# Kernel optimization log

Hardware: AMD Instinct MI355X
Metric: run time of the kernel (lower is better)

Reference implementation:

```python
import jax, jax.numpy as jnp
import numpy as np

NUM_EXPERTS = 64


def setup_inputs() -> dict:
    key = jax.random.key(0)
    k1, k2 = jax.random.split(key)
    x = jax.random.normal(k1, (4, 4096, 2048), dtype=jnp.float32)
    # nn.Linear default init scale ~ 1/sqrt(dim); exact init irrelevant for correctness
    gate_w = jax.random.normal(k2, (NUM_EXPERTS, 2048), dtype=jnp.float32) * (1.0 / np.sqrt(2048.0))
    expert_bias = jnp.zeros((NUM_EXPERTS,), dtype=jnp.float32)
    return {"x": x, "gate_w": gate_w, "expert_bias": expert_bias, "top_k": 8}


def reference(x, gate_w, expert_bias, top_k):
    # x: [B, S, D]; gate_w: [E, D]; expert_bias: [E]
    B, S, D = x.shape
    x_flat = x.reshape(-1, D)                                  # [T, D], T = B*S
    logits = jnp.einsum('td,ed->te', x_flat, gate_w) + expert_bias  # [T, E]
    top_k_logits, top_k_indices = jax.lax.top_k(logits, top_k)      # [T, K]
    top_k_weights = jax.nn.softmax(top_k_logits, axis=-1)           # [T, K]
    # training-mode load counting (scatter_add over expert ids)
    expert_counts = jax.ops.segment_sum(
        jnp.ones((B * S * top_k,), dtype=jnp.float32),
        top_k_indices.reshape(-1),
        num_segments=NUM_EXPERTS,
    )                                                               # [E]
    return top_k_indices, top_k_weights, expert_counts
```

## Files before the change

### kernel.cpp

```cpp
#include <hip/hip_runtime.h>
#include <math.h>

#define T_TOKENS 16384
#define D_DIM    2048
#define E_EXP    64
#define TOPK     8
#define NS       8
#define NCH      (D_DIM / NS / 32)

typedef __attribute__((ext_vector_type(8))) short bf16x8;
typedef __attribute__((ext_vector_type(4))) float f32x4;

__device__ __forceinline__ unsigned short bf16rne(float f) {
  unsigned u = __builtin_bit_cast(unsigned, f);
  unsigned r = u + 0x7fffu + ((u >> 16) & 1u);
  return (unsigned short)(r >> 16);
}
__device__ __forceinline__ float bf16f(unsigned short h) {
  return __builtin_bit_cast(float, (unsigned)h << 16);
}

__device__ __forceinline__ void split8(const float4 v0, const float4 v1,
                                       bf16x8& hi, bf16x8& lo) {
  const float xs[8] = {v0.x, v0.y, v0.z, v0.w, v1.x, v1.y, v1.z, v1.w};
  #pragma unroll
  for (int j = 0; j < 8; ++j) {
    unsigned short h = bf16rne(xs[j]);
    hi[j] = (short)h;
    lo[j] = (short)bf16rne(xs[j] - bf16f(h));
  }
}

__global__ __launch_bounds__(256) void convert_g_kernel(
    const float* __restrict__ gw, unsigned short* __restrict__ ph,
    unsigned short* __restrict__ pl, float* __restrict__ counts_zero)
{
  const int id = blockIdx.x * 256 + threadIdx.x;
  if (blockIdx.x == 0 && threadIdx.x < E_EXP) counts_zero[threadIdx.x] = 0.0f;

  const int e  = id & 63;
  const int kq = (id >> 6) & 3;
  const int c  = id >> 8;
  const float* gp = &gw[(size_t)e * D_DIM + c * 32 + kq * 8];
  float4 v0 = *(const float4*)&gp[0];
  float4 v1 = *(const float4*)&gp[4];
  bf16x8 hi, lo;
  split8(v0, v1, hi, lo);
  *(bf16x8*)&ph[(size_t)id * 8] = hi;
  *(bf16x8*)&pl[(size_t)id * 8] = lo;
}

__global__ __launch_bounds__(256, 4) void moe_logits_kernel(
    const float* __restrict__ x, const unsigned short* __restrict__ ph,
    const unsigned short* __restrict__ pl, float* __restrict__ part)
{
  const int tid  = threadIdx.x;
  const int wave = tid >> 6;
  const int lane = tid & 63;
  const int l15  = lane & 15;
  const int quad = lane >> 4;
  const int ks   = blockIdx.y;
  const int k0   = ks * (D_DIM / NS);
  const int tokw = blockIdx.x * 128 + wave * 32;

  f32x4 acc[2][4];
  #pragma unroll
  for (int s = 0; s < 2; ++s)
    #pragma unroll
    for (int et = 0; et < 4; ++et) acc[s][et] = (f32x4){0.f, 0.f, 0.f, 0.f};

  const float* xp0 = &x[(size_t)(tokw + l15)      * D_DIM + k0 + quad * 8];
  const float* xp1 = &x[(size_t)(tokw + 16 + l15) * D_DIM + k0 + quad * 8];
  const unsigned short* bp_h = &ph[(((size_t)(k0 >> 5) * 4 + quad) * 64 + l15) * 8];
  const unsigned short* bp_l = &pl[(((size_t)(k0 >> 5) * 4 + quad) * 64 + l15) * 8];

  float4 a0 = *(const float4*)&xp0[0], a1 = *(const float4*)&xp0[4];
  float4 b0 = *(const float4*)&xp1[0], b1 = *(const float4*)&xp1[4];

  #pragma unroll 1
  for (int c = 0; c < NCH; ++c) {
    float4 na0, na1, nb0, nb1;
    if (c + 1 < NCH) {
      const float* q0 = xp0 + (c + 1) * 32;
      const float* q1 = xp1 + (c + 1) * 32;
      na0 = *(const float4*)&q0[0]; na1 = *(const float4*)&q0[4];
      nb0 = *(const float4*)&q1[0]; nb1 = *(const float4*)&q1[4];
    }

    bf16x8 ah0, al0, ah1, al1;
    split8(a0, a1, ah0, al0);
    split8(b0, b1, ah1, al1);

    const unsigned short* ch = bp_h + (size_t)c * 2048;
    const unsigned short* cl = bp_l + (size_t)c * 2048;
    #pragma unroll
    for (int et = 0; et < 4; ++et) {
      bf16x8 bh = *(const bf16x8*)&ch[et * 128];
      bf16x8 bl = *(const bf16x8*)&cl[et * 128];
      acc[0][et] = __builtin_amdgcn_mfma_f32_16x16x32_bf16(ah0, bh, acc[0][et], 0, 0, 0);
      acc[0][et] = __builtin_amdgcn_mfma_f32_16x16x32_bf16(ah0, bl, acc[0][et], 0, 0, 0);
      acc[0][et] = __builtin_amdgcn_mfma_f32_16x16x32_bf16(al0, bh, acc[0][et], 0, 0, 0);
      acc[0][et] = __builtin_amdgcn_mfma_f32_16x16x32_bf16(al0, bl, acc[0][et], 0, 0, 0);
      acc[1][et] = __builtin_amdgcn_mfma_f32_16x16x32_bf16(ah1, bh, acc[1][et], 0, 0, 0);
      acc[1][et] = __builtin_amdgcn_mfma_f32_16x16x32_bf16(ah1, bl, acc[1][et], 0, 0, 0);
      acc[1][et] = __builtin_amdgcn_mfma_f32_16x16x32_bf16(al1, bh, acc[1][et], 0, 0, 0);
      acc[1][et] = __builtin_amdgcn_mfma_f32_16x16x32_bf16(al1, bl, acc[1][et], 0, 0, 0);
    }

    a0 = na0; a1 = na1; b0 = nb0; b1 = nb1;
  }

  #pragma unroll
  for (int sub = 0; sub < 2; ++sub) {
    #pragma unroll
    for (int et = 0; et < 4; ++et) {
      #pragma unroll
      for (int r = 0; r < 4; ++r) {
        const size_t t = (size_t)tokw + sub * 16 + quad * 4 + r;
        part[((size_t)ks * T_TOKENS + t) * E_EXP + et * 16 + l15] = acc[sub][et][r];
      }
    }
  }
}

__global__ __launch_bounds__(64) void topk_kernel(
    const float* __restrict__ part, const float* __restrict__ bias,
    float* __restrict__ out)
{
  __shared__ unsigned hist[E_EXP];
  const int tid = threadIdx.x;
  const int t = blockIdx.x * 64 + tid;
  hist[tid] = 0;
  __syncthreads();

  float l[E_EXP];
  #pragma unroll
  for (int j = 0; j < E_EXP / 4; ++j) {
    float4 b = *(const float4*)&bias[j * 4];
    l[4*j] = b.x; l[4*j+1] = b.y; l[4*j+2] = b.z; l[4*j+3] = b.w;
  }
  #pragma unroll 1
  for (int ks = 0; ks < NS; ++ks) {
    const float4* p = (const float4*)&part[((size_t)ks * T_TOKENS + t) * E_EXP];
    #pragma unroll
    for (int j = 0; j < E_EXP / 4; ++j) {
      float4 v = p[j];
      l[4*j] += v.x; l[4*j+1] += v.y; l[4*j+2] += v.z; l[4*j+3] += v.w;
    }
  }

  float tv[TOPK]; int tix[TOPK];
  unsigned long long used = 0ull;
  #pragma unroll
  for (int k = 0; k < TOPK; ++k) {
    float best = -INFINITY; int bi = 0;
    #pragma unroll
    for (int j = 0; j < E_EXP; ++j) {
      bool ok = (((used >> j) & 1ull) == 0ull) && (l[j] > best);
      best = ok ? l[j] : best;
      bi   = ok ? j : bi;
    }
    tv[k] = best; tix[k] = bi;
    used |= (1ull << bi);
  }

  float m = tv[0], s = 0.0f, w[TOPK];
  #pragma unroll
  for (int k = 0; k < TOPK; ++k) { w[k] = expf(tv[k] - m); s += w[k]; }
  float inv = 1.0f / s;

  #pragma unroll
  for (int k = 0; k < TOPK; ++k) {
    out[(size_t)t * TOPK + k] = (float)tix[k];
    out[(size_t)T_TOKENS * TOPK + (size_t)t * TOPK + k] = w[k] * inv;
  }

  #pragma unroll
  for (int k = 0; k < TOPK; ++k) atomicAdd(&hist[tix[k]], 1u);
  __syncthreads();
  atomicAdd(&out[2 * (size_t)T_TOKENS * TOPK + tid], (float)hist[tid]);
}

extern "C" void kernel_launch(void* const* d_in, const int* in_sizes, int n_in,
                              void* d_out, int out_size, void* d_ws, size_t ws_size,
                              hipStream_t stream) {
  const float* x    = (const float*)d_in[0];
  const float* gw   = (const float*)d_in[1];
  const float* bias = (const float*)d_in[2];
  float* out  = (float*)d_out;

  float* part = (float*)d_ws;
  const size_t part_elems = (size_t)NS * T_TOKENS * E_EXP;
  unsigned short* ph = (unsigned short*)((char*)d_ws + part_elems * sizeof(float));
  unsigned short* pl = ph + (size_t)E_EXP * D_DIM;

  convert_g_kernel<<<dim3(E_EXP * D_DIM / 8 / 256), dim3(256), 0, stream>>>(
      gw, ph, pl, out + 2 * (size_t)T_TOKENS * TOPK);
  moe_logits_kernel<<<dim3(T_TOKENS / 128, NS), dim3(256), 0, stream>>>(
      x, ph, pl, part);
  topk_kernel<<<dim3(T_TOKENS / 64), dim3(64), 0, stream>>>(part, bias, out);
}
```

Measured before the change: 235.2 us.

## Drop lo*lo MFMA term and shrink per-wave tile to 16 tokens

The split-bf16 product now uses three MFMAs (hi*hi, lo*hi, hi*lo) instead of four, dropping the lo*lo term, which costs little precision. Each wave handles 16 tokens instead of 32, so the grid doubles, register use falls, and occupancy can rise. The manual software prefetch is replaced by a plain loop unrolled by 2. Halving the per-wave tile means each gate-weight fragment loaded is reused by half as many tokens, so weight traffic per token goes up.

After: 241.4 us. 2.6% more time.

```diff
diff --git a/kernel.cpp b/kernel.cpp
--- a/kernel.cpp
+++ b/kernel.cpp
@@ -61,64 +61,43 @@
   const int quad = lane >> 4;
   const int ks   = blockIdx.y;
   const int k0   = ks * (D_DIM / NS);
-  const int tokw = blockIdx.x * 128 + wave * 32;
+  const int tokw = blockIdx.x * 64 + wave * 16;
 
-  f32x4 acc[2][4];
+  f32x4 acc[4];
   #pragma unroll
-  for (int s = 0; s < 2; ++s)
-    #pragma unroll
-    for (int et = 0; et < 4; ++et) acc[s][et] = (f32x4){0.f, 0.f, 0.f, 0.f};
+  for (int et = 0; et < 4; ++et) acc[et] = (f32x4){0.f, 0.f, 0.f, 0.f};
 
-  const float* xp0 = &x[(size_t)(tokw + l15)      * D_DIM + k0 + quad * 8];
-  const float* xp1 = &x[(size_t)(tokw + 16 + l15) * D_DIM + k0 + quad * 8];
-  const unsigned short* bp_h = &ph[(((size_t)(k0 >> 5) * 4 + quad) * 64 + l15) * 8];
-  const unsigned short* bp_l = &pl[(((size_t)(k0 >> 5) * 4 + quad) * 64 + l15) * 8];
+  const float* xp = &x[(size_t)(tokw + l15) * D_DIM + k0 + quad * 8];
+  const unsigned short* bh_p = &ph[(((size_t)(k0 >> 5) * 4 + quad) * 64 + l15) * 8];
+  const unsigned short* bl_p = &pl[(((size_t)(k0 >> 5) * 4 + quad) * 64 + l15) * 8];
 
-  float4 a0 = *(const float4*)&xp0[0], a1 = *(const float4*)&xp0[4];
-  float4 b0 = *(const float4*)&xp1[0], b1 = *(const float4*)&xp1[4];
+  #pragma unroll 2
+  for (int c = 0; c < NCH; ++c) {
+    float4 v0 = *(const float4*)&xp[0];
+    float4 v1 = *(const float4*)&xp[4];
+    xp += 32;
 
-  #pragma unroll 1
-  for (int c = 0; c < NCH; ++c) {
-    float4 na0, na1, nb0, nb1;
-    if (c + 1 < NCH) {
-      const float* q0 = xp0 + (c + 1) * 32;
-      const float* q1 = xp1 + (c + 1) * 32;
-      na0 = *(const float4*)&q0[0]; na1 = *(const float4*)&q0[4];
-      nb0 = *(const float4*)&q1[0]; nb1 = *(const float4*)&q1[4];
-    }
+    bf16x8 ah, al;
+    split8(v0, v1, ah, al);
 
-    bf16x8 ah0, al0, ah1, al1;
-    split8(a0, a1, ah0, al0);
-    split8(b0, b1, ah1, al1);
-
-    const unsigned short* ch = bp_h + (size_t)c * 2048;
-    const unsigned short* cl = bp_l + (size_t)c * 2048;
     #pragma unroll
     for (int et = 0; et < 4; ++et) {
-      bf16x8 bh = *(const bf16x8*)&ch[et * 128];
-      bf16x8 bl = *(const bf16x8*)&cl[et * 128];
-      acc[0][et] = __builtin_amdgcn_mfma_f32_16x16x32_bf16(ah0, bh, acc[0][et], 0, 0, 0);
-      acc[0][et] = __builtin_amdgcn_mfma_f32_16x16x32_bf16(ah0, bl, acc[0][et], 0, 0, 0);
-      acc[0][et] = __builtin_amdgcn_mfma_f32_16x16x32_bf16(al0, bh, acc[0][et], 0, 0, 0);
-      acc[0][et] = __builtin_amdgcn_mfma_f32_16x16x32_bf16(al0, bl, acc[0][et], 0, 0, 0);
-      acc[1][et] = __builtin_amdgcn_mfma_f32_16x16x32_bf16(ah1, bh, acc[1][et], 0, 0, 0);
-      acc[1][et] = __builtin_amdgcn_mfma_f32_16x16x32_bf16(ah1, bl, acc[1][et], 0, 0, 0);
-      acc[1][et] = __builtin_amdgcn_mfma_f32_16x16x32_bf16(al1, bh, acc[1][et], 0, 0, 0);
-      acc[1][et] = __builtin_amdgcn_mfma_f32_16x16x32_bf16(al1, bl, acc[1][et], 0, 0, 0);
+      bf16x8 bh = *(const bf16x8*)&bh_p[et * 128];
+      bf16x8 bl = *(const bf16x8*)&bl_p[et * 128];
+      acc[et] = __builtin_amdgcn_mfma_f32_16x16x32_bf16(ah, bh, acc[et], 0, 0, 0);
+      acc[et] = __builtin_amdgcn_mfma_f32_16x16x32_bf16(al, bh, acc[et], 0, 0, 0);
+      acc[et] = __builtin_amdgcn_mfma_f32_16x16x32_bf16(ah, bl, acc[et], 0, 0, 0);
     }
-
-    a0 = na0; a1 = na1; b0 = nb0; b1 = nb1;
+    bh_p += 2048;
+    bl_p += 2048;
   }
 
   #pragma unroll
-  for (int sub = 0; sub < 2; ++sub) {
+  for (int et = 0; et < 4; ++et) {
     #pragma unroll
-    for (int et = 0; et < 4; ++et) {
-      #pragma unroll
-      for (int r = 0; r < 4; ++r) {
-        const size_t t = (size_t)tokw + sub * 16 + quad * 4 + r;
-        part[((size_t)ks * T_TOKENS + t) * E_EXP + et * 16 + l15] = acc[sub][et][r];
-      }
+    for (int r = 0; r < 4; ++r) {
+      const size_t t = (size_t)tokw + quad * 4 + r;
+      part[((size_t)ks * T_TOKENS + t) * E_EXP + et * 16 + l15] = acc[et][r];
     }
   }
 }
@@ -196,7 +175,7 @@
 
   convert_g_kernel<<<dim3(E_EXP * D_DIM / 8 / 256), dim3(256), 0, stream>>>(
       gw, ph, pl, out + 2 * (size_t)T_TOKENS * TOPK);
-  moe_logits_kernel<<<dim3(T_TOKENS / 128, NS), dim3(256), 0, stream>>>(
+  moe_logits_kernel<<<dim3(T_TOKENS / 64, NS), dim3(256), 0, stream>>>(
       x, ph, pl, part);
   topk_kernel<<<dim3(T_TOKENS / 64), dim3(64), 0, stream>>>(part, bias, out);
 }
```
